# Optimization experiments

Hardware: AMD Instinct MI355X
Metric: run time of the kernel (lower is better)

The kernel has to match this reference:

```python
import jax, jax.numpy as jnp
import numpy as np

C = 64; NB_ERB = 32; NB_DF = 96; EMB = 256; KT = 2
LSNR_SCALE = 50.0; LSNR_OFFSET = -15.0

def _conv2d(x, w, b, stride=(1, 1)):
    # NCHW conv; freq padding 1, no temporal padding (causal ring buffer handles time)
    out = jax.lax.conv_general_dilated(
        x, w, window_strides=stride, padding=((0, 0), (1, 1)),
        dimension_numbers=('NCHW', 'OIHW', 'NCHW'))
    return out + b[None, :, None, None]


def setup_inputs() -> dict:
    key = jax.random.key(0)
    ks = jax.random.split(key, 32)
    n = lambda i, shape, s=0.05: jax.random.normal(ks[i], shape, dtype=jnp.float32) * s
    return {
        'feat_erb': n(0, (1, 1, 1, NB_ERB), 1.0),
        'feat_spec': n(1, (1, 2, 1, NB_DF), 1.0),
        'buf_erb0': n(2, (1, 1, KT - 1, NB_ERB), 1.0),
        'buf_df0': n(3, (1, 2, KT - 1, NB_DF), 1.0),
        'h_enc': n(4, (1, 1, EMB), 1.0),
        'W_erb0': n(5, (C, 1, KT, 3)), 'b_erb0': n(6, (C,)),
        'W_erb1': n(7, (C, C, 1, 3)), 'b_erb1': n(8, (C,)),
        'W_erb2': n(9, (C, C, 1, 3)), 'b_erb2': n(10, (C,)),
        'W_erb3': n(11, (C, C, 1, 3)), 'b_erb3': n(12, (C,)),
        'W_df0': n(13, (C, 2, KT, 3)), 'b_df0': n(14, (C,)),
        'W_df1': n(15, (C, C, 1, 3)), 'b_df1': n(16, (C,)),
        'W_dffc': n(17, (EMB, C * (NB_DF // 2))), 'b_dffc': n(18, (EMB,)),
        'W_ih': n(19, (3 * EMB, EMB)), 'b_ih': n(20, (3 * EMB,)),
        'W_hh': n(21, (3 * EMB, EMB)), 'b_hh': n(22, (3 * EMB,)),
        'W_lsnr': n(23, (1, EMB)), 'b_lsnr': n(24, (1,)),
    }


def reference(feat_erb, feat_spec, buf_erb0, buf_df0, h_enc,
              W_erb0, b_erb0, W_erb1, b_erb1, W_erb2, b_erb2, W_erb3, b_erb3,
              W_df0, b_df0, W_df1, b_df1, W_dffc, b_dffc,
              W_ih, b_ih, W_hh, b_hh, W_lsnr, b_lsnr):
    relu = jax.nn.relu
    # ERB path: causal conv via explicit ring buffer
    ctx_erb = jnp.concatenate([buf_erb0, feat_erb], axis=2)     # [1,1,KT,32]
    e0 = relu(_conv2d(ctx_erb, W_erb0, b_erb0))                 # [1,C,1,32]
    buf_erb0_new = ctx_erb[:, :, 1:, :]
    e1 = relu(_conv2d(e0, W_erb1, b_erb1, stride=(1, 2)))       # [1,C,1,16]
    e2 = relu(_conv2d(e1, W_erb2, b_erb2, stride=(1, 2)))       # [1,C,1,8]
    e3 = relu(_conv2d(e2, W_erb3, b_erb3, stride=(1, 2)))       # [1,C,1,4]
    # DF path
    ctx_df = jnp.concatenate([buf_df0, feat_spec], axis=2)      # [1,2,KT,96]
    c0 = relu(_conv2d(ctx_df, W_df0, b_df0))                    # [1,C,1,96]
    buf_df0_new = ctx_df[:, :, 1:, :]
    c1 = relu(_conv2d(c0, W_df1, b_df1, stride=(1, 2)))         # [1,C,1,48]
    c1f = jnp.transpose(c1, (0, 2, 3, 1)).reshape(1, 1, -1)     # [1,1,48*C]
    cemb = relu(c1f @ W_dffc.T + b_dffc)                        # [1,1,EMB]
    emb_raw = jnp.transpose(e3, (0, 2, 3, 1)).reshape(1, 1, -1) # [1,1,EMB]
    emb_raw = emb_raw + cemb                                    # combine = add
    # Single-layer GRU step (torch gate semantics)
    x2 = emb_raw[:, 0]                                          # [1,EMB]
    h2 = h_enc[0]                                               # [1,EMB]
    gi = x2 @ W_ih.T + b_ih
    gh = h2 @ W_hh.T + b_hh
    ir, iz, inn = jnp.split(gi, 3, axis=-1)
    hr, hz, hn = jnp.split(gh, 3, axis=-1)
    r = jax.nn.sigmoid(ir + hr)
    z = jax.nn.sigmoid(iz + hz)
    ng = jnp.tanh(inn + r * hn)
    h_new = (1.0 - z) * ng + z * h2                             # [1,EMB]
    emb = h_new[:, None, :]                                     # [1,1,EMB]
    h_enc_new = h_new[None]                                     # [1,1,EMB]
    lsnr = (jax.nn.sigmoid(emb @ W_lsnr.T + b_lsnr) * LSNR_SCALE + LSNR_OFFSET).reshape(1)
    return (e0, e1, e2, e3, emb, c0, lsnr, buf_erb0_new, buf_df0_new, h_enc_new)
```

## Files before the change

kernel.cpp:

```cpp
#include <hip/hip_runtime.h>
#include <math.h>

#define NB_ERB 32
#define NB_DF 96
#define EMB 256

#define OUT_E0      0
#define OUT_E1      2048
#define OUT_E2      3072
#define OUT_E3      3584
#define OUT_EMB     3840
#define OUT_C0      4096
#define OUT_LSNR    10240
#define OUT_BUF_ERB 10241
#define OUT_BUF_DF  10273
#define OUT_HENC    10465

#define WS_PART 0

static __device__ __forceinline__ float sigm(float x) {
    return 1.0f / (1.0f + expf(-x));
}

__global__ __launch_bounds__(256) void ka(
    const float* __restrict__ feat_erb, const float* __restrict__ feat_spec,
    const float* __restrict__ buf_erb0, const float* __restrict__ buf_df0,
    const float* __restrict__ W_erb0, const float* __restrict__ b_erb0,
    const float* __restrict__ W_erb1, const float* __restrict__ b_erb1,
    const float* __restrict__ W_erb2, const float* __restrict__ b_erb2,
    const float* __restrict__ W_erb3, const float* __restrict__ b_erb3,
    const float* __restrict__ W_df0,  const float* __restrict__ b_df0,
    const float* __restrict__ W_df1,  const float* __restrict__ b_df1,
    const float* __restrict__ W_dffc,
    float* __restrict__ out, float* __restrict__ ws)
{
    const int blk = blockIdx.x, t = threadIdx.x;
    __shared__ float sW1[64 * 193];
    __shared__ float sW2[64 * 193];
    __shared__ __align__(16) float sA[2048];
    __shared__ __align__(16) float sB[1024];
    __shared__ float s_c0[192];
    __shared__ float s_c1[64];

    if (blk == 0) {
        const int o = t & 63, wg = t >> 6;
        float4 wbuf[12];

        {
            const float4* W1v = reinterpret_cast<const float4*>(W_erb1);
            #pragma unroll
            for (int j = 0; j < 12; ++j) wbuf[j] = W1v[t + 256 * j];
        }
        {
            const int oc = t >> 2, q = t & 3;
            const float* W = W_erb0 + oc * 6;
            const float b0 = b_erb0[oc];
            #pragma unroll
            for (int m = 0; m < 8; ++m) {
                int w_ = q * 8 + m;
                float a = b0;
                #pragma unroll
                for (int kw = 0; kw < 3; ++kw) {
                    int x = w_ + kw - 1;
                    if (x >= 0 && x < NB_ERB)
                        a += W[kw] * buf_erb0[x] + W[3 + kw] * feat_erb[x];
                }
                float v = fmaxf(a, 0.0f);
                sA[oc * 32 + w_] = v;
                out[OUT_E0 + oc * 32 + w_] = v;
            }
        }
        if (t < 32) out[OUT_BUF_ERB + t] = feat_erb[t];
        {
            #pragma unroll
            for (int j = 0; j < 12; ++j) {
                int k4 = t + 256 * j;
                float* p = &sW1[(k4 / 48) * 193 + (k4 % 48) * 4];
                p[0] = wbuf[j].x; p[1] = wbuf[j].y; p[2] = wbuf[j].z; p[3] = wbuf[j].w;
            }
            const float4* W2v = reinterpret_cast<const float4*>(W_erb2);
            #pragma unroll
            for (int j = 0; j < 12; ++j) wbuf[j] = W2v[t + 256 * j];
        }
        __syncthreads();

        {
            float bias = b_erb1[o];
            float a0 = bias, a1 = bias, a2 = bias, a3 = bias;
            const float* wrow = &sW1[o * 193];
            for (int i = 0; i < 64; ++i) {
                float w0 = wrow[i * 3], w1 = wrow[i * 3 + 1], w2 = wrow[i * 3 + 2];
                const float* e = &sA[i * 32 + wg * 8];
                float em1 = (wg == 0) ? 0.0f : e[-1];
                float4 v0 = *reinterpret_cast<const float4*>(e);
                float4 v1 = *reinterpret_cast<const float4*>(e + 4);
                a0 += w0 * em1  + w1 * v0.x + w2 * v0.y;
                a1 += w0 * v0.y + w1 * v0.z + w2 * v0.w;
                a2 += w0 * v0.w + w1 * v1.x + w2 * v1.y;
                a3 += w0 * v1.y + w1 * v1.z + w2 * v1.w;
            }
            float4 r = make_float4(fmaxf(a0, 0.f), fmaxf(a1, 0.f),
                                   fmaxf(a2, 0.f), fmaxf(a3, 0.f));
            reinterpret_cast<float4*>(&sB[o * 16])[wg] = r;
            reinterpret_cast<float4*>(out + OUT_E1)[o * 4 + wg] = r;
        }
        {
            #pragma unroll
            for (int j = 0; j < 12; ++j) {
                int k4 = t + 256 * j;
                float* p = &sW2[(k4 / 48) * 193 + (k4 % 48) * 4];
                p[0] = wbuf[j].x; p[1] = wbuf[j].y; p[2] = wbuf[j].z; p[3] = wbuf[j].w;
            }
            const float4* W3v = reinterpret_cast<const float4*>(W_erb3);
            #pragma unroll
            for (int j = 0; j < 12; ++j) wbuf[j] = W3v[t + 256 * j];
        }
        __syncthreads();

        {
            float bias = b_erb2[o];
            float a0 = bias, a1 = bias;
            const float* wrow = &sW2[o * 193];
            for (int i = 0; i < 64; ++i) {
                float w0 = wrow[i * 3], w1 = wrow[i * 3 + 1], w2 = wrow[i * 3 + 2];
                const float* e = &sB[i * 16 + wg * 4];
                float em1 = (wg == 0) ? 0.0f : e[-1];
                float4 v = *reinterpret_cast<const float4*>(e);
                a0 += w0 * em1 + w1 * v.x + w2 * v.y;
                a1 += w0 * v.y + w1 * v.z + w2 * v.w;
            }
            a0 = fmaxf(a0, 0.0f); a1 = fmaxf(a1, 0.0f);
            int w = 2 * wg;
            sA[o * 8 + w] = a0; sA[o * 8 + w + 1] = a1;
            out[OUT_E2 + o * 8 + w] = a0; out[OUT_E2 + o * 8 + w + 1] = a1;
        }
        {
            #pragma unroll
            for (int j = 0; j < 12; ++j) {
                int k4 = t + 256 * j;
                float* p = &sW1[(k4 / 48) * 193 + (k4 % 48) * 4];
                p[0] = wbuf[j].x; p[1] = wbuf[j].y; p[2] = wbuf[j].z; p[3] = wbuf[j].w;
            }
        }
        __syncthreads();

        {
            float a = b_erb3[o];
            const float* wrow = &sW1[o * 193];
            for (int i = 0; i < 64; ++i) {
                float w0 = wrow[i * 3], w1 = wrow[i * 3 + 1], w2 = wrow[i * 3 + 2];
                const float* e = &sA[i * 8 + 2 * wg];
                float em1 = (wg == 0) ? 0.0f : e[-1];
                a += w0 * em1 + w1 * e[0] + w2 * e[1];
            }
            out[OUT_E3 + o * 4 + wg] = fmaxf(a, 0.0f);
        }
    } else {
        const int w = blk - 1;
        if (blk == 1 && t < 192) out[OUT_BUF_DF + t] = feat_spec[t];
        if (t < 192) {
            const int i = t & 63, j = t >> 6;
            const int X = 2 * w - 1 + j;
            float v = 0.0f;
            if (X >= 0) {
                float acc = b_df0[i];
                const float* Wp = W_df0 + i * 12;
                #pragma unroll
                for (int c = 0; c < 2; ++c)
                    #pragma unroll
                    for (int kw = 0; kw < 3; ++kw) {
                        int x = X + kw - 1;
                        if (x >= 0 && x < NB_DF) {
                            acc += Wp[c * 6 + kw]     * buf_df0[c * NB_DF + x];
                            acc += Wp[c * 6 + 3 + kw] * feat_spec[c * NB_DF + x];
                        }
                    }
                v = fmaxf(acc, 0.0f);
                if (j >= 1) out[OUT_C0 + i * NB_DF + X] = v;
            }
            s_c0[i * 3 + j] = v;
        }
        __syncthreads();
        const int c = t >> 2, p = t & 3;
        float wloc[48];
        {
            const float4* Wv = reinterpret_cast<const float4*>(W_df1 + c * 192 + p * 48);
            #pragma unroll
            for (int q = 0; q < 12; ++q) {
                float4 v = Wv[q];
                wloc[4 * q] = v.x; wloc[4 * q + 1] = v.y;
                wloc[4 * q + 2] = v.z; wloc[4 * q + 3] = v.w;
            }
        }
        float acc = 0.0f;
        #pragma unroll
        for (int ii = 0; ii < 16; ++ii) {
            int i = p * 16 + ii;
            acc += wloc[ii * 3]     * s_c0[i * 3]
                 + wloc[ii * 3 + 1] * s_c0[i * 3 + 1]
                 + wloc[ii * 3 + 2] * s_c0[i * 3 + 2];
        }
        acc += __shfl_down(acc, 2, 4);
        acc += __shfl_down(acc, 1, 4);
        if (p == 0) s_c1[c] = fmaxf(acc + b_df1[c], 0.0f);
        __syncthreads();
        {
            const float4* Wp = reinterpret_cast<const float4*>(W_dffc + t * 3072 + w * 64);
            float a = 0.0f;
            #pragma unroll
            for (int q = 0; q < 16; ++q) {
                float4 v = Wp[q];
                a += v.x * s_c1[q * 4]     + v.y * s_c1[q * 4 + 1]
                   + v.z * s_c1[q * 4 + 2] + v.w * s_c1[q * 4 + 3];
            }
            ws[WS_PART + w * 256 + t] = a;
        }
    }
}

__global__ __launch_bounds__(256) void kb(
    const float* __restrict__ h_enc, const float* __restrict__ b_dffc,
    const float* __restrict__ W_ih,  const float* __restrict__ b_ih,
    const float* __restrict__ W_hh,  const float* __restrict__ b_hh,
    float* __restrict__ out, const float* __restrict__ ws)
{
    const int t = threadIdx.x, blk = blockIdx.x;
    __shared__ __align__(16) float s_x2[256];
    {
        float acc = b_dffc[t];
        #pragma unroll 8
        for (int w = 0; w < 48; ++w) acc += ws[WS_PART + w * 256 + t];
        float cemb = fmaxf(acc, 0.0f);
        float e3v = out[OUT_E3 + (t & 63) * 4 + (t >> 6)];
        s_x2[t] = e3v + cemb;
    }
    __syncthreads();
    const int wv = t >> 6, lane = t & 63;
    const int o = blk * 4 + wv;
    const float4 xv = *reinterpret_cast<const float4*>(&s_x2[lane * 4]);
    const float4 hv = *reinterpret_cast<const float4*>(h_enc + lane * 4);
    const float4 wir = *reinterpret_cast<const float4*>(W_ih + (o      ) * EMB + lane * 4);
    const float4 wiz = *reinterpret_cast<const float4*>(W_ih + (o + 256) * EMB + lane * 4);
    const float4 win = *reinterpret_cast<const float4*>(W_ih + (o + 512) * EMB + lane * 4);
    const float4 whr = *reinterpret_cast<const float4*>(W_hh + (o      ) * EMB + lane * 4);
    const float4 whz = *reinterpret_cast<const float4*>(W_hh + (o + 256) * EMB + lane * 4);
    const float4 whn = *reinterpret_cast<const float4*>(W_hh + (o + 512) * EMB + lane * 4);
    float air = wir.x * xv.x + wir.y * xv.y + wir.z * xv.z + wir.w * xv.w;
    float aiz = wiz.x * xv.x + wiz.y * xv.y + wiz.z * xv.z + wiz.w * xv.w;
    float ain = win.x * xv.x + win.y * xv.y + win.z * xv.z + win.w * xv.w;
    float ahr = whr.x * hv.x + whr.y * hv.y + whr.z * hv.z + whr.w * hv.w;
    float ahz = whz.x * hv.x + whz.y * hv.y + whz.z * hv.z + whz.w * hv.w;
    float ahn = whn.x * hv.x + whn.y * hv.y + whn.z * hv.z + whn.w * hv.w;
    #pragma unroll
    for (int off = 32; off; off >>= 1) {
        air += __shfl_down(air, off);
        aiz += __shfl_down(aiz, off);
        ain += __shfl_down(ain, off);
        ahr += __shfl_down(ahr, off);
        ahz += __shfl_down(ahz, off);
        ahn += __shfl_down(ahn, off);
    }
    if (lane == 0) {
        float r  = sigm(air + b_ih[o]       + ahr + b_hh[o]);
        float z  = sigm(aiz + b_ih[o + 256] + ahz + b_hh[o + 256]);
        float ng = tanhf(ain + b_ih[o + 512] + r * (ahn + b_hh[o + 512]));
        float h  = (1.0f - z) * ng + z * h_enc[o];
        out[OUT_EMB  + o] = h;
        out[OUT_HENC + o] = h;
    }
}

__global__ __launch_bounds__(256) void kc(
    const float* __restrict__ W_lsnr, const float* __restrict__ b_lsnr,
    float* __restrict__ out)
{
    const int t = threadIdx.x;
    __shared__ float s[4];
    float v = out[OUT_EMB + t] * W_lsnr[t];
    #pragma unroll
    for (int off = 32; off; off >>= 1) v += __shfl_down(v, off);
    if ((t & 63) == 0) s[t >> 6] = v;
    __syncthreads();
    if (t == 0)
        out[OUT_LSNR] = sigm(s[0] + s[1] + s[2] + s[3] + b_lsnr[0]) * 50.0f - 15.0f;
}

extern "C" void kernel_launch(void* const* d_in, const int* in_sizes, int n_in,
                              void* d_out, int out_size, void* d_ws, size_t ws_size,
                              hipStream_t stream) {
    (void)in_sizes; (void)n_in; (void)out_size; (void)ws_size;
    const float* feat_erb  = (const float*)d_in[0];
    const float* feat_spec = (const float*)d_in[1];
    const float* buf_erb0  = (const float*)d_in[2];
    const float* buf_df0   = (const float*)d_in[3];
    const float* h_enc     = (const float*)d_in[4];
    const float* W_erb0    = (const float*)d_in[5];
    const float* b_erb0    = (const float*)d_in[6];
    const float* W_erb1    = (const float*)d_in[7];
    const float* b_erb1    = (const float*)d_in[8];
    const float* W_erb2    = (const float*)d_in[9];
    const float* b_erb2    = (const float*)d_in[10];
    const float* W_erb3    = (const float*)d_in[11];
    const float* b_erb3    = (const float*)d_in[12];
    const float* W_df0     = (const float*)d_in[13];
    const float* b_df0     = (const float*)d_in[14];
    const float* W_df1     = (const float*)d_in[15];
    const float* b_df1     = (const float*)d_in[16];
    const float* W_dffc    = (const float*)d_in[17];
    const float* b_dffc    = (const float*)d_in[18];
    const float* W_ih      = (const float*)d_in[19];
    const float* b_ih      = (const float*)d_in[20];
    const float* W_hh      = (const float*)d_in[21];
    const float* b_hh      = (const float*)d_in[22];
    const float* W_lsnr    = (const float*)d_in[23];
    const float* b_lsnr    = (const float*)d_in[24];
    float* out = (float*)d_out;
    float* ws  = (float*)d_ws;

    hipLaunchKernelGGL(ka, dim3(49), dim3(256), 0, stream,
                       feat_erb, feat_spec, buf_erb0, buf_df0,
                       W_erb0, b_erb0, W_erb1, b_erb1, W_erb2, b_erb2,
                       W_erb3, b_erb3, W_df0, b_df0, W_df1, b_df1,
                       W_dffc, out, ws);
    hipLaunchKernelGGL(kb, dim3(64), dim3(256), 0, stream,
                       h_enc, b_dffc, W_ih, b_ih, W_hh, b_hh, out, ws);
    hipLaunchKernelGGL(kc, dim3(1), dim3(256), 0, stream,
                       W_lsnr, b_lsnr, out);
}
```

Baseline: 125.1 us.

## Move W_hh GEMV into first kernel and fuse lsnr into GRU kernel

Adds 48 extra blocks to the first kernel that compute the hidden-state GRU projection (W_hh·h + b_hh) into workspace, in parallel with the conv/DF work, since it does not depend on those results. The GRU kernel then only does the input projection. The separate lsnr kernel is removed: each GRU block atomically accumulates its partial dot product and the last block to arrive, found by an atomic counter, writes lsnr. This drops one kernel launch and takes the W_hh loads off the critical path, at the cost of atomics and counter reset logic in workspace.

```diff
diff --git a/kernel.cpp b/kernel.cpp
--- a/kernel.cpp
+++ b/kernel.cpp
@@ -17,6 +17,9 @@
 #define OUT_HENC    10465
 
 #define WS_PART 0
+#define WS_GH   12288
+#define WS_CNT  13056
+#define WS_LACC 13057
 
 static __device__ __forceinline__ float sigm(float x) {
     return 1.0f / (1.0f + expf(-x));
@@ -25,6 +28,7 @@
 __global__ __launch_bounds__(256) void ka(
     const float* __restrict__ feat_erb, const float* __restrict__ feat_spec,
     const float* __restrict__ buf_erb0, const float* __restrict__ buf_df0,
+    const float* __restrict__ h_enc,
     const float* __restrict__ W_erb0, const float* __restrict__ b_erb0,
     const float* __restrict__ W_erb1, const float* __restrict__ b_erb1,
     const float* __restrict__ W_erb2, const float* __restrict__ b_erb2,
@@ -32,6 +36,7 @@
     const float* __restrict__ W_df0,  const float* __restrict__ b_df0,
     const float* __restrict__ W_df1,  const float* __restrict__ b_df1,
     const float* __restrict__ W_dffc,
+    const float* __restrict__ W_hh,   const float* __restrict__ b_hh,
     float* __restrict__ out, float* __restrict__ ws)
 {
     const int blk = blockIdx.x, t = threadIdx.x;
@@ -43,6 +48,10 @@
     __shared__ float s_c1[64];
 
     if (blk == 0) {
+        if (t == 0) {
+            ((int*)ws)[WS_CNT] = 0;
+            ws[WS_LACC] = 0.0f;
+        }
         const int o = t & 63, wg = t >> 6;
         float4 wbuf[12];
 
@@ -155,7 +164,7 @@
             }
             out[OUT_E3 + o * 4 + wg] = fmaxf(a, 0.0f);
         }
-    } else {
+    } else if (blk <= 48) {
         const int w = blk - 1;
         if (blk == 1 && t < 192) out[OUT_BUF_DF + t] = feat_spec[t];
         if (t < 192) {
@@ -215,17 +224,37 @@
             }
             ws[WS_PART + w * 256 + t] = a;
         }
+    } else {
+        const int wv = t >> 6, lane = t & 63;
+        const int o0 = (blk - 49) * 16 + wv * 4;
+        const float4 hv = *reinterpret_cast<const float4*>(h_enc + lane * 4);
+        float r[4];
+        #pragma unroll
+        for (int j = 0; j < 4; ++j) {
+            const float4 wr = *reinterpret_cast<const float4*>(W_hh + (o0 + j) * EMB + lane * 4);
+            r[j] = wr.x * hv.x + wr.y * hv.y + wr.z * hv.z + wr.w * hv.w;
+        }
+        #pragma unroll
+        for (int off = 32; off; off >>= 1) {
+            #pragma unroll
+            for (int j = 0; j < 4; ++j) r[j] += __shfl_down(r[j], off);
+        }
+        if (lane == 0) {
+            #pragma unroll
+            for (int j = 0; j < 4; ++j) ws[WS_GH + o0 + j] = r[j] + b_hh[o0 + j];
+        }
     }
 }
 
 __global__ __launch_bounds__(256) void kb(
     const float* __restrict__ h_enc, const float* __restrict__ b_dffc,
     const float* __restrict__ W_ih,  const float* __restrict__ b_ih,
-    const float* __restrict__ W_hh,  const float* __restrict__ b_hh,
-    float* __restrict__ out, const float* __restrict__ ws)
+    const float* __restrict__ W_lsnr, const float* __restrict__ b_lsnr,
+    float* __restrict__ out, float* __restrict__ ws)
 {
     const int t = threadIdx.x, blk = blockIdx.x;
     __shared__ __align__(16) float s_x2[256];
+    __shared__ float s_l[4];
     {
         float acc = b_dffc[t];
         #pragma unroll 8
@@ -238,51 +267,39 @@
     const int wv = t >> 6, lane = t & 63;
     const int o = blk * 4 + wv;
     const float4 xv = *reinterpret_cast<const float4*>(&s_x2[lane * 4]);
-    const float4 hv = *reinterpret_cast<const float4*>(h_enc + lane * 4);
     const float4 wir = *reinterpret_cast<const float4*>(W_ih + (o      ) * EMB + lane * 4);
     const float4 wiz = *reinterpret_cast<const float4*>(W_ih + (o + 256) * EMB + lane * 4);
     const float4 win = *reinterpret_cast<const float4*>(W_ih + (o + 512) * EMB + lane * 4);
-    const float4 whr = *reinterpret_cast<const float4*>(W_hh + (o      ) * EMB + lane * 4);
-    const float4 whz = *reinterpret_cast<const float4*>(W_hh + (o + 256) * EMB + lane * 4);
-    const float4 whn = *reinterpret_cast<const float4*>(W_hh + (o + 512) * EMB + lane * 4);
     float air = wir.x * xv.x + wir.y * xv.y + wir.z * xv.z + wir.w * xv.w;
     float aiz = wiz.x * xv.x + wiz.y * xv.y + wiz.z * xv.z + wiz.w * xv.w;
     float ain = win.x * xv.x + win.y * xv.y + win.z * xv.z + win.w * xv.w;
-    float ahr = whr.x * hv.x + whr.y * hv.y + whr.z * hv.z + whr.w * hv.w;
-    float ahz = whz.x * hv.x + whz.y * hv.y + whz.z * hv.z + whz.w * hv.w;
-    float ahn = whn.x * hv.x + whn.y * hv.y + whn.z * hv.z + whn.w * hv.w;
     #pragma unroll
     for (int off = 32; off; off >>= 1) {
         air += __shfl_down(air, off);
         aiz += __shfl_down(aiz, off);
         ain += __shfl_down(ain, off);
-        ahr += __shfl_down(ahr, off);
-        ahz += __shfl_down(ahz, off);
-        ahn += __shfl_down(ahn, off);
     }
     if (lane == 0) {
-        float r  = sigm(air + b_ih[o]       + ahr + b_hh[o]);
-        float z  = sigm(aiz + b_ih[o + 256] + ahz + b_hh[o + 256]);
-        float ng = tanhf(ain + b_ih[o + 512] + r * (ahn + b_hh[o + 512]));
+        float r  = sigm(air + b_ih[o]       + ws[WS_GH + o]);
+        float z  = sigm(aiz + b_ih[o + 256] + ws[WS_GH + 256 + o]);
+        float ng = tanhf(ain + b_ih[o + 512] + r * ws[WS_GH + 512 + o]);
         float h  = (1.0f - z) * ng + z * h_enc[o];
         out[OUT_EMB  + o] = h;
         out[OUT_HENC + o] = h;
-    }
-}
-
-__global__ __launch_bounds__(256) void kc(
-    const float* __restrict__ W_lsnr, const float* __restrict__ b_lsnr,
-    float* __restrict__ out)
-{
-    const int t = threadIdx.x;
-    __shared__ float s[4];
-    float v = out[OUT_EMB + t] * W_lsnr[t];
-    #pragma unroll
-    for (int off = 32; off; off >>= 1) v += __shfl_down(v, off);
-    if ((t & 63) == 0) s[t >> 6] = v;
+        s_l[wv] = h * W_lsnr[o];
+    }
     __syncthreads();
-    if (t == 0)
-        out[OUT_LSNR] = sigm(s[0] + s[1] + s[2] + s[3] + b_lsnr[0]) * 50.0f - 15.0f;
+    if (t == 0) {
+        float p = s_l[0] + s_l[1] + s_l[2] + s_l[3];
+        atomicAdd(&ws[WS_LACC], p);
+        __threadfence();
+        int old = atomicAdd(&((int*)ws)[WS_CNT], 1);
+        if (old == 63) {
+            __threadfence();
+            float tot = atomicAdd(&ws[WS_LACC], 0.0f);
+            out[OUT_LSNR] = sigm(tot + b_lsnr[0]) * 50.0f - 15.0f;
+        }
+    }
 }
 
 extern "C" void kernel_launch(void* const* d_in, const int* in_sizes, int n_in,
@@ -317,13 +334,11 @@
     float* out = (float*)d_out;
     float* ws  = (float*)d_ws;
 
-    hipLaunchKernelGGL(ka, dim3(49), dim3(256), 0, stream,
-                       feat_erb, feat_spec, buf_erb0, buf_df0,
+    hipLaunchKernelGGL(ka, dim3(97), dim3(256), 0, stream,
+                       feat_erb, feat_spec, buf_erb0, buf_df0, h_enc,
                        W_erb0, b_erb0, W_erb1, b_erb1, W_erb2, b_erb2,
                        W_erb3, b_erb3, W_df0, b_df0, W_df1, b_df1,
-                       W_dffc, out, ws);
+                       W_dffc, W_hh, b_hh, out, ws);
     hipLaunchKernelGGL(kb, dim3(64), dim3(256), 0, stream,
-                       h_enc, b_dffc, W_ih, b_ih, W_hh, b_hh, out, ws);
-    hipLaunchKernelGGL(kc, dim3(1), dim3(256), 0, stream,
-                       W_lsnr, b_lsnr, out);
+                       h_enc, b_dffc, W_ih, b_ih, W_lsnr, b_lsnr, out, ws);
 }
```

Result: slower. 127.8 us (+2.2%).
